# Optimization experiments

Hardware: AMD Instinct MI355X
Metric: run time of the kernel (lower is better)

## Reference

```python
import jax, jax.numpy as jnp
import numpy as np

B, S, D, H = 4, 2048, 1024, 16
DK = D // H

def setup_inputs() -> dict:
    key = jax.random.key(0)
    ks = jax.random.split(key, 11)
    scale = 1.0 / np.sqrt(D)
    inp = {
        'q': jax.random.normal(ks[0], (B, S, D), jnp.float32),
        'k': jax.random.normal(ks[1], (B, S, D), jnp.float32),
        'v': jax.random.normal(ks[2], (B, S, D), jnp.float32),
        'Wq': jax.random.normal(ks[3], (D, D), jnp.float32) * scale,
        'bq': jnp.zeros((D,), jnp.float32),
        'Wk': jax.random.normal(ks[4], (D, D), jnp.float32) * scale,
        'bk': jnp.zeros((D,), jnp.float32),
        'Wv': jax.random.normal(ks[5], (D, D), jnp.float32) * scale,
        'bv': jnp.zeros((D,), jnp.float32),
        'Wo': jax.random.normal(ks[6], (D, D), jnp.float32) * scale,
        'bo': jnp.zeros((D,), jnp.float32),
        # diagonal mask: 0 on the diagonal (self position masked out), 1 elsewhere
        'mask': (1 - jnp.eye(S, dtype=jnp.int32))[None, None, :, :],
    }
    return inp


def reference(q, k, v, Wq, bq, Wk, bk, Wv, bv, Wo, bo, mask):
    def proj(x, W, b):
        # [B,S,D] -> [B,H,S,DK]
        y = x @ W.T + b
        return y.reshape(B, S, H, DK).transpose(0, 2, 1, 3)

    qh = proj(q, Wq, bq)
    kh = proj(k, Wk, bk)
    vh = proj(v, Wv, bv)

    scores = jnp.einsum('bhsd,bhtd->bhst', qh, kh) / jnp.sqrt(jnp.float32(DK))
    scores = jnp.where(mask == 0, jnp.finfo(scores.dtype).min, scores)
    attn = jax.nn.softmax(scores, axis=-1)  # dropout is identity in eval mode
    out = jnp.einsum('bhst,bhtd->bhsd', attn, vh)
    out = out.transpose(0, 2, 1, 3).reshape(B, S, D)
    return out @ Wo.T + bo
```

## Files before the change

### kernel.cpp

```cpp
#include <hip/hip_runtime.h>
#include <stdint.h>

#define S_LEN 2048
#define D_DIM 1024
#define NB 4
#define NH 16
#define DKH 64
#define M_ROWS (NB * S_LEN)
#define PLD 72

typedef float  f32x4 __attribute__((ext_vector_type(4)));
typedef short  s16x8 __attribute__((ext_vector_type(8)));
typedef unsigned short u16;
typedef u16    u16x4 __attribute__((ext_vector_type(4)));

#define AS1 __attribute__((address_space(1)))
#define AS3 __attribute__((address_space(3)))

__device__ __forceinline__ void gload16(const u16* g, u16* l) {
    __builtin_amdgcn_global_load_lds((const AS1 void*)g, (AS3 void*)l, 16, 0, 0);
}

__device__ __forceinline__ u16 f2bf(float f) {
    uint32_t u = __builtin_bit_cast(uint32_t, f);
    return (u16)((u + 0x7fffu + ((u >> 16) & 1u)) >> 16);
}
__device__ __forceinline__ u16 f2bf_cheap(float f) {
    uint32_t u = __builtin_bit_cast(uint32_t, f);
    return (u16)((u + 0x8000u) >> 16);
}

__global__ __launch_bounds__(256) void conv_kernel(const float* __restrict__ src,
                                                   u16* __restrict__ dst, int n)
{
    int i = (blockIdx.x * 256 + threadIdx.x) * 8;
    if (i + 8 > n) return;
    f32x4 a = *(const f32x4*)(src + i);
    f32x4 b = *(const f32x4*)(src + i + 4);
    s16x8 r;
#pragma unroll
    for (int j = 0; j < 4; ++j) r[j]     = (short)f2bf(a[j]);
#pragma unroll
    for (int j = 0; j < 4; ++j) r[j + 4] = (short)f2bf(b[j]);
    *(s16x8*)(dst + i) = r;
}

__global__ __launch_bounds__(256) void conv2_kernel(const float* __restrict__ a,
                                                    const float* __restrict__ b,
                                                    u16* __restrict__ da,
                                                    u16* __restrict__ db)
{
    const float* src = blockIdx.z ? b : a;
    u16* dst        = blockIdx.z ? db : da;
    int i = (blockIdx.x * 256 + threadIdx.x) * 8;
    f32x4 lo = *(const f32x4*)(src + i);
    f32x4 hi = *(const f32x4*)(src + i + 4);
    s16x8 r;
#pragma unroll
    for (int j = 0; j < 4; ++j) r[j]     = (short)f2bf(lo[j]);
#pragma unroll
    for (int j = 0; j < 4; ++j) r[j + 4] = (short)f2bf(hi[j]);
    *(s16x8*)(dst + i) = r;
}

__global__ __launch_bounds__(256) void conv3_kernel(const float* __restrict__ a,
                                                    const float* __restrict__ b,
                                                    const float* __restrict__ c,
                                                    u16* __restrict__ dst)
{
    const int z = blockIdx.z;
    const float* src = (z == 0) ? a : (z == 1) ? b : c;
    int i = (blockIdx.x * 256 + threadIdx.x) * 8;
    f32x4 lo = *(const f32x4*)(src + i);
    f32x4 hi = *(const f32x4*)(src + i + 4);
    s16x8 r;
#pragma unroll
    for (int j = 0; j < 4; ++j) r[j]     = (short)f2bf(lo[j]);
#pragma unroll
    for (int j = 0; j < 4; ++j) r[j + 4] = (short)f2bf(hi[j]);
    *(s16x8*)(dst + (size_t)z * (D_DIM * D_DIM) + i) = r;
}

__device__ __forceinline__ void stage_tile(const u16* __restrict__ X,
                                           const u16* __restrict__ Wt,
                                           int m0, int n0, int k0,
                                           u16* As, u16* Bs, int tid, int wv)
{
#pragma unroll
    for (int i = 0; i < 4; ++i) {
        const int c   = tid + i * 256;
        const int row = c >> 3;
        const int sg  = (c & 7) ^ (row & 7);
        const int lb  = (i * 256 + wv * 64) * 8;
        gload16(&X [(size_t)(m0 + row) * D_DIM + k0 + sg * 8], &As[lb]);
        gload16(&Wt[(size_t)(n0 + row) * D_DIM + k0 + sg * 8], &Bs[lb]);
    }
}

__device__ __forceinline__ void compute_tile(const u16* As, const u16* Bs,
                                             f32x4 acc[4][4],
                                             int wm, int wn, int ln, int quad, int l7)
{
#pragma unroll
    for (int ks = 0; ks < 2; ++ks) {
        const int sA = ((ks * 4 + quad) ^ l7) * 8;
        s16x8 af[4], bfr[4];
#pragma unroll
        for (int t = 0; t < 4; ++t) {
            af[t]  = *(const s16x8*)&As[(wm * 64 + t * 16 + ln) * 64 + sA];
            bfr[t] = *(const s16x8*)&Bs[(wn * 64 + t * 16 + ln) * 64 + sA];
        }
#pragma unroll
        for (int tM = 0; tM < 4; ++tM)
#pragma unroll
            for (int tN = 0; tN < 4; ++tN)
                acc[tM][tN] = __builtin_amdgcn_mfma_f32_16x16x32_bf16(
                    af[tM], bfr[tN], acc[tM][tN], 0, 0, 0);
    }
}

__device__ __forceinline__ void gemm128_body(const u16* __restrict__ X,
                                             const u16* __restrict__ Wt,
                                             int m0, int n0,
                                             u16* As, u16* Bs,
                                             f32x4 acc[4][4])
{
    const int tid  = threadIdx.x;
    const int wv   = tid >> 6;
    const int lane = tid & 63;
    const int ln   = lane & 15;
    const int quad = lane >> 4;
    const int wm   = wv >> 1;
    const int wn   = wv & 1;
    const int l7   = ln & 7;

    for (int k0 = 0; k0 < D_DIM; k0 += 64) {
        __syncthreads();
        stage_tile(X, Wt, m0, n0, k0, As, Bs, tid, wv);
        __syncthreads();
        compute_tile(As, Bs, acc, wm, wn, ln, quad, l7);
    }
}

__device__ __forceinline__ void gemm128_dbuf(const u16* __restrict__ X,
                                             const u16* __restrict__ Wt,
                                             int m0, int n0,
                                             u16* As0, u16* Bs0,
                                             u16* As1, u16* Bs1,
                                             f32x4 acc[4][4])
{
    const int tid  = threadIdx.x;
    const int wv   = tid >> 6;
    const int lane = tid & 63;
    const int ln   = lane & 15;
    const int quad = lane >> 4;
    const int wm   = wv >> 1;
    const int wn   = wv & 1;
    const int l7   = ln & 7;

    stage_tile(X, Wt, m0, n0, 0, As0, Bs0, tid, wv);
    __syncthreads();
    for (int t = 0; t < 16; t += 2) {
        stage_tile(X, Wt, m0, n0, (t + 1) * 64, As1, Bs1, tid, wv);
        compute_tile(As0, Bs0, acc, wm, wn, ln, quad, l7);
        __syncthreads();
        if (t + 2 < 16)
            stage_tile(X, Wt, m0, n0, (t + 2) * 64, As0, Bs0, tid, wv);
        compute_tile(As1, Bs1, acc, wm, wn, ln, quad, l7);
        __syncthreads();
    }
}

__global__ __launch_bounds__(256) void qk_kernel(
    const u16* __restrict__ xq, const u16* __restrict__ xk,
    const u16* __restrict__ Wb,
    const float* __restrict__ bq, const float* __restrict__ bk,
    u16* __restrict__ Qh, u16* __restrict__ Kh)
{
    __shared__ __attribute__((aligned(16))) u16 As[128 * 64];
    __shared__ __attribute__((aligned(16))) u16 Bs[128 * 64];

    const int mode = blockIdx.z;
    const u16* X        = mode ? xk : xq;
    const u16* Wt       = Wb + (size_t)mode * (D_DIM * D_DIM);
    const float* bias   = mode ? bk : bq;
    u16* dst            = mode ? Kh : Qh;
    const float qscale  = mode ? 1.0f : 0.18033688011112042f;

    const int lin = blockIdx.y * 8 + blockIdx.x;
    const int swz = (lin & 7) * 64 + (lin >> 3);
    const int n0  = (swz & 7) * 128;
    const int m0  = (swz >> 3) * 128;

    f32x4 zero = {0.f, 0.f, 0.f, 0.f};
    f32x4 acc[4][4];
#pragma unroll
    for (int i = 0; i < 4; ++i)
#pragma unroll
        for (int j = 0; j < 4; ++j) acc[i][j] = zero;

    gemm128_body(X, Wt, m0, n0, As, Bs, acc);

    const int tid  = threadIdx.x;
    const int wv   = tid >> 6;
    const int lane = tid & 63;
    const int ln   = lane & 15;
    const int quad = lane >> 4;
    const int wm   = wv >> 1;
    const int wn   = wv & 1;

#pragma unroll
    for (int tM = 0; tM < 4; ++tM) {
#pragma unroll
        for (int tN = 0; tN < 4; ++tN) {
            const int ng = n0 + wn * 64 + tN * 16 + ln;
            const float bf32 = bias[ng];
            const int h  = ng >> 6;
            const int dk = ng & 63;
            const int mbase = m0 + wm * 64 + tM * 16 + quad * 4;
            const int b = mbase >> 11;
            const int s = mbase & 2047;
#pragma unroll
            for (int r = 0; r < 4; ++r)
                dst[((size_t)(b * NH + h) * S_LEN + (s + r)) * DKH + dk] =
                    f2bf((acc[tM][tN][r] + bf32) * qscale);
        }
    }
}

__global__ __launch_bounds__(256) void vproj_kernel(
    const u16* __restrict__ xv, const u16* __restrict__ Wv2,
    const float* __restrict__ bv, u16* __restrict__ Vt)
{
    __shared__ __attribute__((aligned(16))) u16 As0[128 * 64];
    __shared__ __attribute__((aligned(16))) u16 Bs0[128 * 64];
    __shared__ __attribute__((aligned(16))) u16 As1[128 * 64];
    __shared__ __attribute__((aligned(16))) u16 Bs1[128 * 64];

    const int lin = blockIdx.y * 8 + blockIdx.x;
    const int swz = (lin & 7) * 64 + (lin >> 3);
    const int n0  = (swz & 7) * 128;
    const int m0  = (swz >> 3) * 128;

    f32x4 zero = {0.f, 0.f, 0.f, 0.f};
    f32x4 acc[4][4];
#pragma unroll
    for (int i = 0; i < 4; ++i)
#pragma unroll
        for (int j = 0; j < 4; ++j) acc[i][j] = zero;

    gemm128_dbuf(xv, Wv2, m0, n0, As0, Bs0, As1, Bs1, acc);

    const int tid  = threadIdx.x;
    const int wv   = tid >> 6;
    const int lane = tid & 63;
    const int ln   = lane & 15;
    const int quad = lane >> 4;
    const int wm   = wv >> 1;
    const int wn   = wv & 1;

#pragma unroll
    for (int tM = 0; tM < 4; ++tM) {
#pragma unroll
        for (int tN = 0; tN < 4; ++tN) {
            const int ng = n0 + wn * 64 + tN * 16 + ln;
            const float bf32 = bv[ng];
            const int h  = ng >> 6;
            const int dk = ng & 63;
            const int mbase = m0 + wm * 64 + tM * 16 + quad * 4;
            const int b = mbase >> 11;
            const int s = mbase & 2047;
            u16x4 pk;
#pragma unroll
            for (int r = 0; r < 4; ++r) pk[r] = f2bf(acc[tM][tN][r] + bf32);
            *(u16x4*)&Vt[((size_t)((b * NH + h) * DKH + dk)) * S_LEN + s] = pk;
        }
    }
}

__global__ __launch_bounds__(256) void attn_kernel(
    const u16* __restrict__ Qh, const u16* __restrict__ Kh,
    const u16* __restrict__ Vt, u16* __restrict__ ctx)
{
    __shared__ __attribute__((aligned(16))) u16 Ks[64 * 64];
    __shared__ __attribute__((aligned(16))) u16 Vs[64 * 64];
    __shared__ __attribute__((aligned(16))) u16 QPs[64 * PLD];

    const int tid  = threadIdx.x;
    const int wv   = tid >> 6;
    const int lane = tid & 63;
    const int ln   = lane & 15;
    const int quad = lane >> 4;
    const int l7   = ln & 7;

    const int lin = blockIdx.y * 32 + blockIdx.x;
    const int xcd = lin & 7;
    const int t_  = lin >> 3;
    const int bh  = xcd * 8 + (t_ >> 5);
    const int q0  = (t_ & 31) * 64;

    const size_t qkbase = (size_t)bh * S_LEN * DKH;
    const size_t vbase  = (size_t)bh * DKH * S_LEN;

#pragma unroll
    for (int i = 0; i < 2; ++i) {
        const int c = tid + i * 256, row = c >> 3;
        const int sg = (c & 7) ^ (row & 7);
        gload16(&Qh[qkbase + (size_t)(q0 + row) * DKH + sg * 8],
                &QPs[(i * 256 + wv * 64) * 8]);
    }
    __syncthreads();

    s16x8 aq[2];
#pragma unroll
    for (int ks = 0; ks < 2; ++ks)
        aq[ks] = *(const s16x8*)&QPs[(wv * 16 + ln) * 64 + (((ks * 4 + quad) ^ l7) * 8)];

    float l_part[4] = {0.f, 0.f, 0.f, 0.f};
    f32x4 zero = {0.f, 0.f, 0.f, 0.f};
    f32x4 o_acc[4] = {zero, zero, zero, zero};

    const int rbase = q0 + wv * 16 + quad * 4;
    const int rowA = wv * 16 + ln;
    const int rotA = (((rowA >> 2) & 7)) * 8;
    const int rotW = ((4 * wv + quad) & 7) * 8;

    for (int kb = 0; kb < S_LEN; kb += 64) {
        __syncthreads();
#pragma unroll
        for (int i = 0; i < 2; ++i) {
            const int c = tid + i * 256, row = c >> 3;
            const int sg = (c & 7) ^ (row & 7);
            const int lb = (i * 256 + wv * 64) * 8;
            gload16(&Kh[qkbase + (size_t)(kb + row) * DKH + sg * 8], &Ks[lb]);
            gload16(&Vt[vbase + (size_t)row * S_LEN + kb + sg * 8], &Vs[lb]);
        }
        __syncthreads();

        f32x4 sf[4];
#pragma unroll
        for (int nt = 0; nt < 4; ++nt) {
            f32x4 acc = zero;
#pragma unroll
            for (int ks = 0; ks < 2; ++ks) {
                s16x8 bk_ = *(const s16x8*)&Ks[(nt * 16 + ln) * 64 + (((ks * 4 + quad) ^ l7) * 8)];
                acc = __builtin_amdgcn_mfma_f32_16x16x32_bf16(aq[ks], bk_, acc, 0, 0, 0);
            }
            sf[nt] = acc;
        }

        if (kb == q0) {
#pragma unroll
            for (int nt = 0; nt < 4; ++nt)
#pragma unroll
                for (int r = 0; r < 4; ++r) {
                    float p = __builtin_amdgcn_exp2f(sf[nt][r]);
                    if (rbase + r == kb + nt * 16 + ln) p = 0.f;
                    sf[nt][r] = p;
                    l_part[r] += p;
                }
        } else {
#pragma unroll
            for (int nt = 0; nt < 4; ++nt)
#pragma unroll
                for (int r = 0; r < 4; ++r) {
                    float p = __builtin_amdgcn_exp2f(sf[nt][r]);
                    sf[nt][r] = p;
                    l_part[r] += p;
                }
        }

#pragma unroll
        for (int nt = 0; nt < 4; ++nt)
#pragma unroll
            for (int r = 0; r < 4; ++r) {
                int row  = wv * 16 + quad * 4 + r;
                int col  = ((nt * 16 + ln) + rotW) & 63;
                QPs[row * PLD + col] = f2bf_cheap(sf[nt][r]);
            }

#pragma unroll
        for (int ks = 0; ks < 2; ++ks) {
            int colA = ((ks * 32 + quad * 8) + rotA) & 63;
            s16x8 ap = *(const s16x8*)&QPs[rowA * PLD + colA];
#pragma unroll
            for (int nt = 0; nt < 4; ++nt) {
                s16x8 bvv = *(const s16x8*)&Vs[(nt * 16 + ln) * 64 + (((ks * 4 + quad) ^ l7) * 8)];
                o_acc[nt] = __builtin_amdgcn_mfma_f32_16x16x32_bf16(ap, bvv, o_acc[nt], 0, 0, 0);
            }
        }
    }

#pragma unroll
    for (int r = 0; r < 4; ++r) {
#pragma unroll
        for (int off = 1; off < 16; off <<= 1)
            l_part[r] += __shfl_xor(l_part[r], off, 16);
    }

    const int b = bh >> 4;
    const int h = bh & 15;
#pragma unroll
    for (int nt = 0; nt < 4; ++nt) {
#pragma unroll
        for (int r = 0; r < 4; ++r) {
            float val = o_acc[nt][r] / l_part[r];
            int sg = q0 + wv * 16 + quad * 4 + r;
            ctx[((size_t)b * S_LEN + sg) * D_DIM + h * DKH + nt * 16 + ln] = f2bf(val);
        }
    }
}

__global__ __launch_bounds__(256) void oproj128_kernel(
    const u16* __restrict__ ctx, const u16* __restrict__ WoB,
    const float* __restrict__ bo, float* __restrict__ out, float sentinel)
{
    __shared__ __attribute__((aligned(16))) u16 As0[128 * 64];
    __shared__ __attribute__((aligned(16))) u16 Bs0[128 * 64];
    __shared__ __attribute__((aligned(16))) u16 As1[128 * 64];
    __shared__ __attribute__((aligned(16))) u16 Bs1[128 * 64];

    const int lin = blockIdx.y * 8 + blockIdx.x;
    const int swz = (lin & 7) * 64 + (lin >> 3);
    const int n0  = (swz & 7) * 128;
    const int m0  = (swz >> 3) * 128;

    f32x4 zero = {0.f, 0.f, 0.f, 0.f};
    f32x4 acc[4][4];
#pragma unroll
    for (int i = 0; i < 4; ++i)
#pragma unroll
        for (int j = 0; j < 4; ++j) acc[i][j] = zero;

    gemm128_dbuf(ctx, WoB, m0, n0, As0, Bs0, As1, Bs1, acc);

    const int tid  = threadIdx.x;
    const int wv   = tid >> 6;
    const int lane = tid & 63;
    const int ln   = lane & 15;
    const int quad = lane >> 4;
    const int wm   = wv >> 1;
    const int wn   = wv & 1;

#pragma unroll
    for (int tM = 0; tM < 4; ++tM) {
#pragma unroll
        for (int tN = 0; tN < 4; ++tN) {
            const int ng = n0 + wn * 64 + tN * 16 + ln;
            const float bf32 = bo[ng];
            const int mbase = m0 + wm * 64 + tM * 16 + quad * 4;
#pragma unroll
            for (int r = 0; r < 4; ++r) {
                float val = acc[tM][tN][r] + bf32;
                if (mbase + r == 0 && ng == 0) val += sentinel;
                out[(size_t)(mbase + r) * D_DIM + ng] = val;
            }
        }
    }
}

extern "C" void kernel_launch(void* const* d_in, const int* in_sizes, int n_in,
                              void* d_out, int out_size, void* d_ws, size_t ws_size,
                              hipStream_t stream)
{
    const float* q  = (const float*)d_in[0];
    const float* k  = (const float*)d_in[1];
    const float* v  = (const float*)d_in[2];
    const float* Wq = (const float*)d_in[3];
    const float* bq = (const float*)d_in[4];
    const float* Wk = (const float*)d_in[5];
    const float* bk = (const float*)d_in[6];
    const float* Wv = (const float*)d_in[7];
    const float* bv = (const float*)d_in[8];
    const float* Wo = (const float*)d_in[9];
    const float* bo = (const float*)d_in[10];

    const size_t headSz = (size_t)NB * NH * S_LEN * DKH;
    const int    WN     = D_DIM * D_DIM;
    u16* Qh  = (u16*)d_ws;
    u16* Kh  = Qh + headSz;
    u16* Vt  = Kh + headSz;
    u16* ctx = Vt + headSz;
    u16* Wb  = (u16*)d_out;
    u16* xk  = Wb + 3 * WN;
    u16* WoB = Qh;
    float* out = (float*)d_out;

    float sentinel = 0.f;
    {
        const int expect[12] = {8388608, 8388608, 8388608, 1048576, 1024, 1048576,
                                1024, 1048576, 1024, 1048576, 1024, 4194304};
        bool ok = (n_in == 12);
        for (int i = 0; ok && i < 12; ++i) ok = (in_sizes[i] == expect[i]);
        if (!ok)                               sentinel = 1000.f;
        else if (ws_size < 4 * headSz * 2)     sentinel = 2000.f;
        else if (out_size != (int)headSz)      sentinel = 3000.f;
    }

    conv3_kernel<<<dim3(WN / 2048, 1, 3), 256, 0, stream>>>(Wq, Wk, Wv, Wb);

    conv_kernel<<<dim3((int)(headSz / 2048)), 256, 0, stream>>>(v, ctx, (int)headSz);
    vproj_kernel<<<dim3(8, 64), 256, 0, stream>>>(ctx, Wb + 2 * WN, bv, Vt);

    conv2_kernel<<<dim3((int)(headSz / 2048), 1, 2), 256, 0, stream>>>(q, k, ctx, xk);
    qk_kernel<<<dim3(8, 64, 2), 256, 0, stream>>>(ctx, xk, Wb, bq, bk, Qh, Kh);

    attn_kernel<<<dim3(S_LEN / 64, NB * NH), 256, 0, stream>>>(Qh, Kh, Vt, ctx);

    conv_kernel<<<dim3(WN / 2048), 256, 0, stream>>>(Wo, WoB, WN);

    oproj128_kernel<<<dim3(8, 64), 256, 0, stream>>>(ctx, WoB, bo, out, sentinel);
}
```

Measured before the change: 386.0 us.

## Use 32x32x16 MFMA in attention with 128-row query tiles; drop GEMM block swizzle

The attention kernel now has each block handle 128 query rows, with each wave owning 32 rows. It switches from 16x16x32 to 32x32x16 bf16 MFMA for both QK^T and PV, which halves K/V reloads per query row and improves MFMA efficiency. The final normalization uses a reciprocal instead of a division. Separately, the projection GEMMs drop their XCD-aware block-index swizzle in favour of plain blockIdx mapping, which may hurt L2 locality. The attention grid halves to 1024 blocks, and register pressure rises from the 16-element accumulators and l_part arrays, so occupancy may drop.

```diff
diff --git a/kernel.cpp b/kernel.cpp
--- a/kernel.cpp
+++ b/kernel.cpp
@@ -9,10 +9,11 @@
 #define M_ROWS (NB * S_LEN)
 #define PLD 72
 
-typedef float  f32x4 __attribute__((ext_vector_type(4)));
-typedef short  s16x8 __attribute__((ext_vector_type(8)));
+typedef float  f32x4  __attribute__((ext_vector_type(4)));
+typedef float  f32x16 __attribute__((ext_vector_type(16)));
+typedef short  s16x8  __attribute__((ext_vector_type(8)));
 typedef unsigned short u16;
-typedef u16    u16x4 __attribute__((ext_vector_type(4)));
+typedef u16    u16x4  __attribute__((ext_vector_type(4)));
 
 #define AS1 __attribute__((address_space(1)))
 #define AS3 __attribute__((address_space(3)))
@@ -187,10 +188,8 @@
     u16* dst            = mode ? Kh : Qh;
     const float qscale  = mode ? 1.0f : 0.18033688011112042f;
 
-    const int lin = blockIdx.y * 8 + blockIdx.x;
-    const int swz = (lin & 7) * 64 + (lin >> 3);
-    const int n0  = (swz & 7) * 128;
-    const int m0  = (swz >> 3) * 128;
+    const int n0 = blockIdx.x * 128;
+    const int m0 = blockIdx.y * 128;
 
     f32x4 zero = {0.f, 0.f, 0.f, 0.f};
     f32x4 acc[4][4];
@@ -237,10 +236,8 @@
     __shared__ __attribute__((aligned(16))) u16 As1[128 * 64];
     __shared__ __attribute__((aligned(16))) u16 Bs1[128 * 64];
 
-    const int lin = blockIdx.y * 8 + blockIdx.x;
-    const int swz = (lin & 7) * 64 + (lin >> 3);
-    const int n0  = (swz & 7) * 128;
-    const int m0  = (swz >> 3) * 128;
+    const int n0 = blockIdx.x * 128;
+    const int m0 = blockIdx.y * 128;
 
     f32x4 zero = {0.f, 0.f, 0.f, 0.f};
     f32x4 acc[4][4];
@@ -284,26 +281,25 @@
 {
     __shared__ __attribute__((aligned(16))) u16 Ks[64 * 64];
     __shared__ __attribute__((aligned(16))) u16 Vs[64 * 64];
-    __shared__ __attribute__((aligned(16))) u16 QPs[64 * PLD];
+    __shared__ __attribute__((aligned(16))) u16 QPs[128 * PLD];
 
     const int tid  = threadIdx.x;
     const int wv   = tid >> 6;
     const int lane = tid & 63;
-    const int ln   = lane & 15;
-    const int quad = lane >> 4;
-    const int l7   = ln & 7;
-
-    const int lin = blockIdx.y * 32 + blockIdx.x;
+    const int l31  = lane & 31;
+    const int hl   = lane >> 5;
+
+    const int lin = blockIdx.y * 16 + blockIdx.x;
     const int xcd = lin & 7;
     const int t_  = lin >> 3;
-    const int bh  = xcd * 8 + (t_ >> 5);
-    const int q0  = (t_ & 31) * 64;
+    const int bh  = xcd * 8 + (t_ >> 4);
+    const int q0  = (t_ & 15) * 128;
 
     const size_t qkbase = (size_t)bh * S_LEN * DKH;
     const size_t vbase  = (size_t)bh * DKH * S_LEN;
 
 #pragma unroll
-    for (int i = 0; i < 2; ++i) {
+    for (int i = 0; i < 4; ++i) {
         const int c = tid + i * 256, row = c >> 3;
         const int sg = (c & 7) ^ (row & 7);
         gload16(&Qh[qkbase + (size_t)(q0 + row) * DKH + sg * 8],
@@ -311,19 +307,25 @@
     }
     __syncthreads();
 
-    s16x8 aq[2];
-#pragma unroll
-    for (int ks = 0; ks < 2; ++ks)
-        aq[ks] = *(const s16x8*)&QPs[(wv * 16 + ln) * 64 + (((ks * 4 + quad) ^ l7) * 8)];
-
-    float l_part[4] = {0.f, 0.f, 0.f, 0.f};
-    f32x4 zero = {0.f, 0.f, 0.f, 0.f};
-    f32x4 o_acc[4] = {zero, zero, zero, zero};
-
-    const int rbase = q0 + wv * 16 + quad * 4;
-    const int rowA = wv * 16 + ln;
-    const int rotA = (((rowA >> 2) & 7)) * 8;
-    const int rotW = ((4 * wv + quad) & 7) * 8;
+    s16x8 aq[4];
+#pragma unroll
+    for (int dsl = 0; dsl < 4; ++dsl) {
+        const int row  = wv * 32 + l31;
+        const int slot = dsl * 2 + hl;
+        aq[dsl] = *(const s16x8*)&QPs[row * 64 + ((slot ^ (row & 7)) * 8)];
+    }
+
+    float l_part[16];
+#pragma unroll
+    for (int j = 0; j < 16; ++j) l_part[j] = 0.f;
+    f32x16 o_acc[2];
+#pragma unroll
+    for (int t = 0; t < 2; ++t)
+#pragma unroll
+        for (int j = 0; j < 16; ++j) o_acc[t][j] = 0.f;
+
+    const int diag_kb = q0 + (wv & 2) * 32;
+    const int qrl = wv * 32 + 4 * hl;
 
     for (int kb = 0; kb < S_LEN; kb += 64) {
         __syncthreads();
@@ -337,76 +339,70 @@
         }
         __syncthreads();
 
-        f32x4 sf[4];
-#pragma unroll
-        for (int nt = 0; nt < 4; ++nt) {
-            f32x4 acc = zero;
-#pragma unroll
-            for (int ks = 0; ks < 2; ++ks) {
-                s16x8 bk_ = *(const s16x8*)&Ks[(nt * 16 + ln) * 64 + (((ks * 4 + quad) ^ l7) * 8)];
-                acc = __builtin_amdgcn_mfma_f32_16x16x32_bf16(aq[ks], bk_, acc, 0, 0, 0);
+#pragma unroll
+        for (int kt = 0; kt < 2; ++kt) {
+            f32x16 sf;
+#pragma unroll
+            for (int j = 0; j < 16; ++j) sf[j] = 0.f;
+#pragma unroll
+            for (int dsl = 0; dsl < 4; ++dsl) {
+                const int row  = kt * 32 + l31;
+                const int slot = dsl * 2 + hl;
+                s16x8 bk_ = *(const s16x8*)&Ks[row * 64 + ((slot ^ (row & 7)) * 8)];
+                sf = __builtin_amdgcn_mfma_f32_32x32x16_bf16(aq[dsl], bk_, sf, 0, 0, 0);
             }
-            sf[nt] = acc;
-        }
-
-        if (kb == q0) {
-#pragma unroll
-            for (int nt = 0; nt < 4; ++nt)
-#pragma unroll
-                for (int r = 0; r < 4; ++r) {
-                    float p = __builtin_amdgcn_exp2f(sf[nt][r]);
-                    if (rbase + r == kb + nt * 16 + ln) p = 0.f;
-                    sf[nt][r] = p;
-                    l_part[r] += p;
+            if (kb == diag_kb) {
+#pragma unroll
+                for (int j = 0; j < 16; ++j) {
+                    float p = __builtin_amdgcn_exp2f(sf[j]);
+                    const int qr = qrl + (j & 3) + 8 * (j >> 2);
+                    if (q0 + qr == kb + kt * 32 + l31) p = 0.f;
+                    l_part[j] += p;
+                    QPs[qr * PLD + kt * 32 + l31] = f2bf_cheap(p);
                 }
-        } else {
-#pragma unroll
-            for (int nt = 0; nt < 4; ++nt)
-#pragma unroll
-                for (int r = 0; r < 4; ++r) {
-                    float p = __builtin_amdgcn_exp2f(sf[nt][r]);
-                    sf[nt][r] = p;
-                    l_part[r] += p;
+            } else {
+#pragma unroll
+                for (int j = 0; j < 16; ++j) {
+                    float p = __builtin_amdgcn_exp2f(sf[j]);
+                    const int qr = qrl + (j & 3) + 8 * (j >> 2);
+                    l_part[j] += p;
+                    QPs[qr * PLD + kt * 32 + l31] = f2bf_cheap(p);
                 }
-        }
-
-#pragma unroll
-        for (int nt = 0; nt < 4; ++nt)
-#pragma unroll
-            for (int r = 0; r < 4; ++r) {
-                int row  = wv * 16 + quad * 4 + r;
-                int col  = ((nt * 16 + ln) + rotW) & 63;
-                QPs[row * PLD + col] = f2bf_cheap(sf[nt][r]);
             }
-
-#pragma unroll
-        for (int ks = 0; ks < 2; ++ks) {
-            int colA = ((ks * 32 + quad * 8) + rotA) & 63;
-            s16x8 ap = *(const s16x8*)&QPs[rowA * PLD + colA];
-#pragma unroll
-            for (int nt = 0; nt < 4; ++nt) {
-                s16x8 bvv = *(const s16x8*)&Vs[(nt * 16 + ln) * 64 + (((ks * 4 + quad) ^ l7) * 8)];
-                o_acc[nt] = __builtin_amdgcn_mfma_f32_16x16x32_bf16(ap, bvv, o_acc[nt], 0, 0, 0);
+        }
+
+#pragma unroll
+        for (int ksl = 0; ksl < 4; ++ksl) {
+            const int rowA = wv * 32 + l31;
+            s16x8 ap = *(const s16x8*)&QPs[rowA * PLD + ksl * 16 + hl * 8];
+#pragma unroll
+            for (int dt = 0; dt < 2; ++dt) {
+                const int rowB = dt * 32 + l31;
+                const int slot = ksl * 2 + hl;
+                s16x8 bv_ = *(const s16x8*)&Vs[rowB * 64 + ((slot ^ (rowB & 7)) * 8)];
+                o_acc[dt] = __builtin_amdgcn_mfma_f32_32x32x16_bf16(ap, bv_, o_acc[dt], 0, 0, 0);
             }
         }
     }
 
 #pragma unroll
-    for (int r = 0; r < 4; ++r) {
-#pragma unroll
-        for (int off = 1; off < 16; off <<= 1)
-            l_part[r] += __shfl_xor(l_part[r], off, 16);
+    for (int j = 0; j < 16; ++j) {
+#pragma unroll
+        for (int off = 1; off < 32; off <<= 1)
+            l_part[j] += __shfl_xor(l_part[j], off, 64);
+        l_part[j] = __builtin_amdgcn_rcpf(l_part[j]);
     }
 
     const int b = bh >> 4;
     const int h = bh & 15;
 #pragma unroll
-    for (int nt = 0; nt < 4; ++nt) {
-#pragma unroll
-        for (int r = 0; r < 4; ++r) {
-            float val = o_acc[nt][r] / l_part[r];
-            int sg = q0 + wv * 16 + quad * 4 + r;
-            ctx[((size_t)b * S_LEN + sg) * D_DIM + h * DKH + nt * 16 + ln] = f2bf(val);
+    for (int dt = 0; dt < 2; ++dt) {
+#pragma unroll
+        for (int j = 0; j < 16; ++j) {
+            const int qr = q0 + qrl + (j & 3) + 8 * (j >> 2);
+            const int d  = dt * 32 + l31;
+            float val = o_acc[dt][j] * l_part[j];
+            ctx[((size_t)b * S_LEN + qr) * D_DIM + h * DKH + d] = f2bf(val);
         }
     }
 }
@@ -420,10 +416,8 @@
     __shared__ __attribute__((aligned(16))) u16 As1[128 * 64];
     __shared__ __attribute__((aligned(16))) u16 Bs1[128 * 64];
 
-    const int lin = blockIdx.y * 8 + blockIdx.x;
-    const int swz = (lin & 7) * 64 + (lin >> 3);
-    const int n0  = (swz & 7) * 128;
-    const int m0  = (swz >> 3) * 128;
+    const int n0 = blockIdx.x * 128;
+    const int m0 = blockIdx.y * 128;
 
     f32x4 zero = {0.f, 0.f, 0.f, 0.f};
     f32x4 acc[4][4];
@@ -505,7 +499,7 @@
     conv2_kernel<<<dim3((int)(headSz / 2048), 1, 2), 256, 0, stream>>>(q, k, ctx, xk);
     qk_kernel<<<dim3(8, 64, 2), 256, 0, stream>>>(ctx, xk, Wb, bq, bk, Qh, Kh);
 
-    attn_kernel<<<dim3(S_LEN / 64, NB * NH), 256, 0, stream>>>(Qh, Kh, Vt, ctx);
+    attn_kernel<<<dim3(S_LEN / 128, NB * NH), 256, 0, stream>>>(Qh, Kh, Vt, ctx);
 
     conv_kernel<<<dim3(WN / 2048), 256, 0, stream>>>(Wo, WoB, WN);
 
```

Result: slower. 405.1 us (+5.0%).
